# Kernel tuning notes

Measured on AMD Instinct MI355X. Metric: run time of the kernel, lower is better.

The kernel has to match this reference:

```python
import jax, jax.numpy as jnp
import numpy as np

N_NODES = 100000
N_EDGES = 1600000
D_FEAT = 32


def setup_inputs() -> dict:
    key = jax.random.key(0)
    k1, k2, k3 = jax.random.split(key, 3)
    hidden = jax.random.normal(k1, (N_NODES, D_FEAT), dtype=jnp.float32)
    src = jax.random.randint(k2, (N_EDGES,), 0, N_NODES, dtype=jnp.int64)
    dst = jax.random.randint(k3, (N_EDGES,), 0, N_NODES, dtype=jnp.int64)
    return {"hidden": hidden, "src": src, "dst": dst}


def reference(hidden, src, dst):
    # msg_gcn: per-edge message = source node feature  -> gather hidden[src]
    # reduce_gcn: sum of mailbox over incoming edges   -> segment_sum by dst
    # apply_gcn: hidden <- reduce (identity copy)
    # Nodes with no in-edges get 0 (DGL leaves them unchanged only if never
    # reduced; with sum-reduce semantics on the mailbox, isolated nodes keep
    # old hidden in DGL — but update_all with a UDF reduce only touches nodes
    # with incoming edges, so we replicate that: keep old value where in-degree==0.
    msg_sum = jax.ops.segment_sum(hidden[src], dst, num_segments=N_NODES)  # [N, D]
    in_deg = jax.ops.segment_sum(jnp.ones((src.shape[0],), dtype=jnp.float32), dst,
                                 num_segments=N_NODES)  # [N]
    has_in = (in_deg > 0)[:, None]  # [N, 1]
    new_hidden = jnp.where(has_in, msg_sum, hidden)
    return new_hidden
```

## Files before the change

kernel.cpp:

```cpp
#include <hip/hip_runtime.h>

#define D_FEAT 32
#define NB_SHIFT 7
#define NODES_PER_BIN 128
#define MAX_BINS 800
#define EBLOCKS 256
#define ETHREADS 1024
#define CAP 2292
#define FT 512
#define EITER 2
#define GITER 2

__global__ void __launch_bounds__(ETHREADS)
fusedfill_kernel(const int* __restrict__ src, const int* __restrict__ dst,
                 int* __restrict__ cur, int* __restrict__ bucket,
                 int n_edges, int nbins, int chunk) {
    __shared__ int h[MAX_BINS];
    __shared__ int obase[MAX_BINS];
    for (int i = threadIdx.x; i < nbins; i += ETHREADS) h[i] = 0;
    __syncthreads();
    int e0 = blockIdx.x * chunk;
    int e1 = min(e0 + chunk, n_edges);
    int nfull = (e1 - e0) >> 2;
    const int4* d4 = (const int4*)(dst + e0);
    const int4* s4 = (const int4*)(src + e0);
    int4 dv[EITER], sv[EITER], rv[EITER];
    #pragma unroll
    for (int it = 0; it < EITER; ++it) {
        int i = threadIdx.x + it * ETHREADS;
        if (i < nfull) {
            int4 d = d4[i];
            dv[it] = d;
            sv[it] = s4[i];
            rv[it].x = atomicAdd(&h[d.x >> NB_SHIFT], 1);
            rv[it].y = atomicAdd(&h[d.y >> NB_SHIFT], 1);
            rv[it].z = atomicAdd(&h[d.z >> NB_SHIFT], 1);
            rv[it].w = atomicAdd(&h[d.w >> NB_SHIFT], 1);
        }
    }
    int erem = e0 + (nfull << 2) + threadIdx.x;
    int drem = 0, srem = 0, rrem = -1;
    if (erem < e1) {
        drem = dst[erem];
        srem = src[erem];
        rrem = atomicAdd(&h[drem >> NB_SHIFT], 1);
    }
    __syncthreads();
    for (int i = threadIdx.x; i < nbins; i += ETHREADS) {
        int c = h[i];
        if (c > 0) {
            int s = atomicAdd(&cur[i], c);
            obase[i] = (s + c <= CAP) ? (i * CAP + s) : -1;
        } else {
            obase[i] = -1;
        }
    }
    __syncthreads();
    #pragma unroll
    for (int it = 0; it < EITER; ++it) {
        int i = threadIdx.x + it * ETHREADS;
        if (i < nfull) {
            int4 d = dv[it], s = sv[it], r = rv[it];
            int b, ob;
            b = d.x >> NB_SHIFT; ob = obase[b];
            if (ob >= 0) bucket[ob + r.x] = ((d.x & (NODES_PER_BIN - 1)) << 17) | s.x;
            b = d.y >> NB_SHIFT; ob = obase[b];
            if (ob >= 0) bucket[ob + r.y] = ((d.y & (NODES_PER_BIN - 1)) << 17) | s.y;
            b = d.z >> NB_SHIFT; ob = obase[b];
            if (ob >= 0) bucket[ob + r.z] = ((d.z & (NODES_PER_BIN - 1)) << 17) | s.z;
            b = d.w >> NB_SHIFT; ob = obase[b];
            if (ob >= 0) bucket[ob + r.w] = ((d.w & (NODES_PER_BIN - 1)) << 17) | s.w;
        }
    }
    if (rrem >= 0) {
        int b = drem >> NB_SHIFT;
        int ob = obase[b];
        if (ob >= 0) bucket[ob + rrem] = ((drem & (NODES_PER_BIN - 1)) << 17) | srem;
    }
}

__global__ void __launch_bounds__(FT)
sortgather_kernel(const float* __restrict__ hidden,
                  const int* __restrict__ bucket,
                  const int* __restrict__ cur,
                  float* __restrict__ out, int n_nodes) {
    __shared__ int stageB[CAP];
    __shared__ int cnt[NODES_PER_BIN];
    __shared__ int base[NODES_PER_BIN];
    __shared__ int sc[NODES_PER_BIN];
    int bin = blockIdx.x;
    int t = threadIdx.x;
    int m = min(cur[bin], CAP);
    int p0 = bin * CAP;
    if (t < NODES_PER_BIN) cnt[t] = 0;
    __syncthreads();
    int nfull = m >> 2;
    const int4* b4 = (const int4*)(bucket + p0);
    int4 vv[GITER], rk[GITER];
    #pragma unroll
    for (int it = 0; it < GITER; ++it) {
        int i = t + it * FT;
        if (i < nfull) {
            int4 v = b4[i];
            vv[it] = v;
            rk[it].x = atomicAdd(&cnt[v.x >> 17], 1);
            rk[it].y = atomicAdd(&cnt[v.y >> 17], 1);
            rk[it].z = atomicAdd(&cnt[v.z >> 17], 1);
            rk[it].w = atomicAdd(&cnt[v.w >> 17], 1);
        }
    }
    int irem = (nfull << 2) + t;
    int vrem = 0, rkrem = -1;
    if (irem < m) {
        vrem = bucket[p0 + irem];
        rkrem = atomicAdd(&cnt[vrem >> 17], 1);
    }
    __syncthreads();
    if (t < NODES_PER_BIN) sc[t] = cnt[t];
    __syncthreads();
    for (int off = 1; off < NODES_PER_BIN; off <<= 1) {
        int v = (t >= off && t < NODES_PER_BIN) ? sc[t - off] : 0;
        __syncthreads();
        if (t < NODES_PER_BIN) sc[t] += v;
        __syncthreads();
    }
    if (t < NODES_PER_BIN) base[t] = sc[t] - cnt[t];
    __syncthreads();
    #pragma unroll
    for (int it = 0; it < GITER; ++it) {
        int i = t + it * FT;
        if (i < nfull) {
            int4 v = vv[it], r = rk[it];
            stageB[base[v.x >> 17] + r.x] = v.x & 0x1FFFF;
            stageB[base[v.y >> 17] + r.y] = v.y & 0x1FFFF;
            stageB[base[v.z >> 17] + r.z] = v.z & 0x1FFFF;
            stageB[base[v.w >> 17] + r.w] = v.w & 0x1FFFF;
        }
    }
    if (rkrem >= 0)
        stageB[base[vrem >> 17] + rkrem] = vrem & 0x1FFFF;
    __syncthreads();
    int gg = t >> 3;
    int l8 = t & 7;
    const float4* h4 = (const float4*)hidden;
    float4* o4 = (float4*)out;
    int nbase = bin << NB_SHIFT;
    for (int ln = gg; ln < NODES_PER_BIN; ln += FT / 8) {
        int node = nbase + ln;
        if (node >= n_nodes) break;
        int c = cnt[ln];
        float4 a0 = make_float4(0.f, 0.f, 0.f, 0.f);
        if (c == 0) {
            o4[(size_t)node * 8 + l8] = h4[(size_t)node * 8 + l8];
            continue;
        }
        float4 a1 = make_float4(0.f, 0.f, 0.f, 0.f);
        int p = base[ln];
        int e = p + c;
        for (; p + 4 <= e; p += 4) {
            int v0 = stageB[p + 0], v1 = stageB[p + 1];
            int v2 = stageB[p + 2], v3 = stageB[p + 3];
            float4 x0 = h4[(size_t)v0 * 8 + l8];
            float4 x1 = h4[(size_t)v1 * 8 + l8];
            float4 x2 = h4[(size_t)v2 * 8 + l8];
            float4 x3 = h4[(size_t)v3 * 8 + l8];
            a0.x += x0.x; a0.y += x0.y; a0.z += x0.z; a0.w += x0.w;
            a1.x += x1.x; a1.y += x1.y; a1.z += x1.z; a1.w += x1.w;
            a0.x += x2.x; a0.y += x2.y; a0.z += x2.z; a0.w += x2.w;
            a1.x += x3.x; a1.y += x3.y; a1.z += x3.z; a1.w += x3.w;
        }
        if (p + 2 <= e) {
            int v0 = stageB[p + 0], v1 = stageB[p + 1];
            float4 x0 = h4[(size_t)v0 * 8 + l8];
            float4 x1 = h4[(size_t)v1 * 8 + l8];
            a0.x += x0.x; a0.y += x0.y; a0.z += x0.z; a0.w += x0.w;
            a1.x += x1.x; a1.y += x1.y; a1.z += x1.z; a1.w += x1.w;
            p += 2;
        }
        if (p < e) {
            float4 x0 = h4[(size_t)stageB[p] * 8 + l8];
            a0.x += x0.x; a0.y += x0.y; a0.z += x0.z; a0.w += x0.w;
        }
        a0.x += a1.x; a0.y += a1.y; a0.z += a1.z; a0.w += a1.w;
        o4[(size_t)node * 8 + l8] = a0;
    }
}

extern "C" void kernel_launch(void* const* d_in, const int* in_sizes, int n_in,
                              void* d_out, int out_size, void* d_ws, size_t ws_size,
                              hipStream_t stream) {
    const float* hidden = (const float*)d_in[0];
    const int* src = (const int*)d_in[1];
    const int* dst = (const int*)d_in[2];
    float* out = (float*)d_out;
    int n_nodes = in_sizes[0] / D_FEAT;
    int n_edges = in_sizes[1];
    int nbins = (n_nodes + NODES_PER_BIN - 1) >> NB_SHIFT;
    int chunk = (((n_edges + EBLOCKS - 1) / EBLOCKS) + 3) & ~3;

    int* cur = (int*)d_ws;
    int* bucket = (int*)((char*)d_ws + 3200);

    hipMemsetAsync(cur, 0, 3200, stream);
    fusedfill_kernel<<<EBLOCKS, ETHREADS, 0, stream>>>(src, dst, cur, bucket,
                                                       n_edges, nbins, chunk);
    sortgather_kernel<<<nbins, FT, 0, stream>>>(hidden, bucket, cur, out, n_nodes);
}
```

Baseline: 56.08 us.

## Sort bin edges by source tile and gather tile-by-tile in lockstep

Bin entries are now sorted by a composite key of destination node and source-index tile (8 tiles of 16K nodes), not by destination node alone. The gather loop walks the tiles in order, with a block barrier after each tile, so all threads in a block read hidden rows from the same source range at the same time to improve cache locality. The 128-entry shared-memory scan is replaced by a 1024-key wavefront-shuffle scan. In exchange each thread handles exactly two nodes with less unrolling, and the barriers per tile can stall warps whose edge counts are unbalanced.

```diff
diff --git a/kernel.cpp b/kernel.cpp
--- a/kernel.cpp
+++ b/kernel.cpp
@@ -10,6 +10,11 @@
 #define FT 512
 #define EITER 2
 #define GITER 2
+#define NTILES 8
+#define TSHIFT 14
+#define NKEYS (NODES_PER_BIN * NTILES)
+
+#define KEY(v) ((((v) >> 17) << 3) | (((v) >> TSHIFT) & (NTILES - 1)))
 
 __global__ void __launch_bounds__(ETHREADS)
 fusedfill_kernel(const int* __restrict__ src, const int* __restrict__ dst,
@@ -85,14 +90,14 @@
                   const int* __restrict__ cur,
                   float* __restrict__ out, int n_nodes) {
     __shared__ int stageB[CAP];
-    __shared__ int cnt[NODES_PER_BIN];
-    __shared__ int base[NODES_PER_BIN];
-    __shared__ int sc[NODES_PER_BIN];
+    __shared__ int cnt[NKEYS];
+    __shared__ int base[NKEYS];
+    __shared__ int wsum[8];
     int bin = blockIdx.x;
     int t = threadIdx.x;
     int m = min(cur[bin], CAP);
     int p0 = bin * CAP;
-    if (t < NODES_PER_BIN) cnt[t] = 0;
+    for (int i = t; i < NKEYS; i += FT) cnt[i] = 0;
     __syncthreads();
     int nfull = m >> 2;
     const int4* b4 = (const int4*)(bucket + p0);
@@ -103,86 +108,106 @@
         if (i < nfull) {
             int4 v = b4[i];
             vv[it] = v;
-            rk[it].x = atomicAdd(&cnt[v.x >> 17], 1);
-            rk[it].y = atomicAdd(&cnt[v.y >> 17], 1);
-            rk[it].z = atomicAdd(&cnt[v.z >> 17], 1);
-            rk[it].w = atomicAdd(&cnt[v.w >> 17], 1);
+            rk[it].x = atomicAdd(&cnt[KEY(v.x)], 1);
+            rk[it].y = atomicAdd(&cnt[KEY(v.y)], 1);
+            rk[it].z = atomicAdd(&cnt[KEY(v.z)], 1);
+            rk[it].w = atomicAdd(&cnt[KEY(v.w)], 1);
         }
     }
     int irem = (nfull << 2) + t;
     int vrem = 0, rkrem = -1;
     if (irem < m) {
         vrem = bucket[p0 + irem];
-        rkrem = atomicAdd(&cnt[vrem >> 17], 1);
-    }
-    __syncthreads();
-    if (t < NODES_PER_BIN) sc[t] = cnt[t];
-    __syncthreads();
-    for (int off = 1; off < NODES_PER_BIN; off <<= 1) {
-        int v = (t >= off && t < NODES_PER_BIN) ? sc[t - off] : 0;
-        __syncthreads();
-        if (t < NODES_PER_BIN) sc[t] += v;
-        __syncthreads();
-    }
-    if (t < NODES_PER_BIN) base[t] = sc[t] - cnt[t];
+        rkrem = atomicAdd(&cnt[KEY(vrem)], 1);
+    }
+    __syncthreads();
+    int c0 = cnt[2 * t], c1 = cnt[2 * t + 1];
+    int s = c0 + c1;
+    int lane = t & 63, w = t >> 6;
+    int pre = s;
+    for (int off = 1; off < 64; off <<= 1) {
+        int x = __shfl_up(pre, off, 64);
+        if (lane >= off) pre += x;
+    }
+    if (lane == 63) wsum[w] = pre;
+    __syncthreads();
+    if (t < 64) {
+        int x = (lane < 8) ? wsum[lane] : 0;
+        int p2 = x;
+        for (int off = 1; off < 8; off <<= 1) {
+            int y = __shfl_up(p2, off, 64);
+            if (lane >= off) p2 += y;
+        }
+        if (lane < 8) wsum[lane] = p2 - x;
+    }
+    __syncthreads();
+    int excl = pre - s + wsum[w];
+    base[2 * t] = excl;
+    base[2 * t + 1] = excl + c0;
     __syncthreads();
     #pragma unroll
     for (int it = 0; it < GITER; ++it) {
         int i = t + it * FT;
         if (i < nfull) {
             int4 v = vv[it], r = rk[it];
-            stageB[base[v.x >> 17] + r.x] = v.x & 0x1FFFF;
-            stageB[base[v.y >> 17] + r.y] = v.y & 0x1FFFF;
-            stageB[base[v.z >> 17] + r.z] = v.z & 0x1FFFF;
-            stageB[base[v.w >> 17] + r.w] = v.w & 0x1FFFF;
+            stageB[base[KEY(v.x)] + r.x] = v.x & 0x1FFFF;
+            stageB[base[KEY(v.y)] + r.y] = v.y & 0x1FFFF;
+            stageB[base[KEY(v.z)] + r.z] = v.z & 0x1FFFF;
+            stageB[base[KEY(v.w)] + r.w] = v.w & 0x1FFFF;
         }
     }
     if (rkrem >= 0)
-        stageB[base[vrem >> 17] + rkrem] = vrem & 0x1FFFF;
+        stageB[base[KEY(vrem)] + rkrem] = vrem & 0x1FFFF;
     __syncthreads();
     int gg = t >> 3;
     int l8 = t & 7;
     const float4* h4 = (const float4*)hidden;
     float4* o4 = (float4*)out;
     int nbase = bin << NB_SHIFT;
-    for (int ln = gg; ln < NODES_PER_BIN; ln += FT / 8) {
-        int node = nbase + ln;
-        if (node >= n_nodes) break;
-        int c = cnt[ln];
-        float4 a0 = make_float4(0.f, 0.f, 0.f, 0.f);
-        if (c == 0) {
-            o4[(size_t)node * 8 + l8] = h4[(size_t)node * 8 + l8];
-            continue;
-        }
-        float4 a1 = make_float4(0.f, 0.f, 0.f, 0.f);
-        int p = base[ln];
-        int e = p + c;
-        for (; p + 4 <= e; p += 4) {
-            int v0 = stageB[p + 0], v1 = stageB[p + 1];
-            int v2 = stageB[p + 2], v3 = stageB[p + 3];
-            float4 x0 = h4[(size_t)v0 * 8 + l8];
-            float4 x1 = h4[(size_t)v1 * 8 + l8];
-            float4 x2 = h4[(size_t)v2 * 8 + l8];
-            float4 x3 = h4[(size_t)v3 * 8 + l8];
+    int ln0 = gg, ln1 = gg + 64;
+    float4 a0 = make_float4(0.f, 0.f, 0.f, 0.f);
+    float4 a1 = make_float4(0.f, 0.f, 0.f, 0.f);
+    int tot0 = 0, tot1 = 0;
+    for (int tile = 0; tile < NTILES; ++tile) {
+        int k0 = (ln0 << 3) | tile;
+        int p = base[k0];
+        int e = p + cnt[k0];
+        tot0 += cnt[k0];
+        for (; p + 2 <= e; p += 2) {
+            float4 x0 = h4[(size_t)stageB[p] * 8 + l8];
+            float4 x1 = h4[(size_t)stageB[p + 1] * 8 + l8];
             a0.x += x0.x; a0.y += x0.y; a0.z += x0.z; a0.w += x0.w;
+            a0.x += x1.x; a0.y += x1.y; a0.z += x1.z; a0.w += x1.w;
+        }
+        if (p < e) {
+            float4 x0 = h4[(size_t)stageB[p] * 8 + l8];
+            a0.x += x0.x; a0.y += x0.y; a0.z += x0.z; a0.w += x0.w;
+        }
+        int k1 = (ln1 << 3) | tile;
+        p = base[k1];
+        e = p + cnt[k1];
+        tot1 += cnt[k1];
+        for (; p + 2 <= e; p += 2) {
+            float4 x0 = h4[(size_t)stageB[p] * 8 + l8];
+            float4 x1 = h4[(size_t)stageB[p + 1] * 8 + l8];
+            a1.x += x0.x; a1.y += x0.y; a1.z += x0.z; a1.w += x0.w;
             a1.x += x1.x; a1.y += x1.y; a1.z += x1.z; a1.w += x1.w;
-            a0.x += x2.x; a0.y += x2.y; a0.z += x2.z; a0.w += x2.w;
-            a1.x += x3.x; a1.y += x3.y; a1.z += x3.z; a1.w += x3.w;
-        }
-        if (p + 2 <= e) {
-            int v0 = stageB[p + 0], v1 = stageB[p + 1];
-            float4 x0 = h4[(size_t)v0 * 8 + l8];
-            float4 x1 = h4[(size_t)v1 * 8 + l8];
-            a0.x += x0.x; a0.y += x0.y; a0.z += x0.z; a0.w += x0.w;
-            a1.x += x1.x; a1.y += x1.y; a1.z += x1.z; a1.w += x1.w;
-            p += 2;
         }
         if (p < e) {
             float4 x0 = h4[(size_t)stageB[p] * 8 + l8];
-            a0.x += x0.x; a0.y += x0.y; a0.z += x0.z; a0.w += x0.w;
-        }
-        a0.x += a1.x; a0.y += a1.y; a0.z += a1.z; a0.w += a1.w;
-        o4[(size_t)node * 8 + l8] = a0;
+            a1.x += x0.x; a1.y += x0.y; a1.z += x0.z; a1.w += x0.w;
+        }
+        __syncthreads();
+    }
+    int node0 = nbase + ln0;
+    if (node0 < n_nodes) {
+        if (tot0 == 0) a0 = h4[(size_t)node0 * 8 + l8];
+        o4[(size_t)node0 * 8 + l8] = a0;
+    }
+    int node1 = nbase + ln1;
+    if (node1 < n_nodes) {
+        if (tot1 == 0) a1 = h4[(size_t)node1 * 8 + l8];
+        o4[(size_t)node1 * 8 + l8] = a1;
     }
 }
 
```

Measured after the change: 54.65 us. 1.03x faster.
